# Optimization experiments

Measured on AMD Instinct MI355X. Metric: run time of the kernel, lower is better.

The kernel has to match this reference:

```python
import jax, jax.numpy as jnp
import numpy as np

B, S, D_IN, D_HID, D_OUT = 8, 2048, 1024, 1024, 1024


def setup_inputs() -> dict:
    key = jax.random.key(0)
    ks = jax.random.split(key, 11)
    def lin(kw, kb, fan_in, fan_out):
        bound = 1.0 / np.sqrt(fan_in)
        W = jax.random.uniform(kw, (fan_out, fan_in), minval=-bound, maxval=bound, dtype=jnp.float32)
        b = jax.random.uniform(kb, (fan_out,), minval=-bound, maxval=bound, dtype=jnp.float32)
        return W, b
    Wq, bq = lin(ks[0], ks[1], D_IN, D_HID)
    Wk, bk = lin(ks[2], ks[3], D_IN, D_HID)
    Wv, bv = lin(ks[4], ks[5], D_IN, D_HID)
    Wo, bo = lin(ks[6], ks[7], D_HID, D_OUT)
    gamma = jnp.ones((D_OUT,), jnp.float32)
    beta = jnp.zeros((D_OUT,), jnp.float32)
    x = jax.random.normal(ks[8], (B, S, D_IN), dtype=jnp.float32)
    return {"x": x, "Wq": Wq, "bq": bq, "Wk": Wk, "bk": bk,
            "Wv": Wv, "bv": bv, "Wo": Wo, "bo": bo,
            "gamma": gamma, "beta": beta}


def _layer_norm(x, gamma, beta, eps=1e-5):
    mu = jnp.mean(x, axis=-1, keepdims=True)
    var = jnp.var(x, axis=-1, keepdims=True)
    return (x - mu) * jax.lax.rsqrt(var + eps) * gamma + beta


def reference(x, Wq, bq, Wk, bk, Wv, bv, Wo, bo, gamma, beta):
    q = jnp.einsum('bsd,hd->bsh', x, Wq) + bq   # [B,S,H]
    k = jnp.einsum('bsd,hd->bsh', x, Wk) + bk
    v = jnp.einsum('bsd,hd->bsh', x, Wv) + bv
    scale = 1.0 / jnp.sqrt(jnp.float32(D_HID))
    scores = jnp.einsum('bqh,bkh->bqk', q, k) * scale  # [B,S,S]
    attn = jax.nn.softmax(scores, axis=-1)
    weighted = jnp.einsum('bqk,bkh->bqh', attn, v)     # [B,S,H]
    out = jnp.einsum('bsh,oh->bso', weighted, Wo) + bo # [B,S,O]
    return _layer_norm(out + x, gamma, beta)
```

## Files before the change

### kernel.cpp

```cpp
#include <hip/hip_runtime.h>
#include <hip/hip_bf16.h>
#include <math.h>


typedef __bf16 bf16;
typedef unsigned char u8;
typedef __attribute__((ext_vector_type(8))) __bf16 bf16x8;
typedef __attribute__((ext_vector_type(4))) __bf16 bf16x4;
typedef __attribute__((ext_vector_type(8))) int i32x8;
typedef __attribute__((ext_vector_type(16))) float f32x16;

__device__ __forceinline__ void async16(const u8* g, u8* l) {
    __builtin_amdgcn_global_load_lds(
        (const __attribute__((address_space(1))) void*)g,
        (__attribute__((address_space(3))) void*)l, 16, 0, 0);
}

#define WAITCNT_VM(n) __builtin_amdgcn_s_waitcnt((15 << 8) | (7 << 4) | (n))

__device__ __forceinline__ u8 to_fp8(float v) {
    return (u8)(__builtin_amdgcn_cvt_pk_fp8_f32(v, v, 0, 0) & 0xFF);
}

__global__ __launch_bounds__(256) void cast_f32_fp8(
    const float* __restrict__ in, u8* __restrict__ out, int n)
{
    int i = (blockIdx.x * 256 + threadIdx.x) * 8;
    if (i >= n) return;
    float4 a = *(const float4*)(in + i);
    float4 b = *(const float4*)(in + i + 4);
    int lo = __builtin_amdgcn_cvt_pk_fp8_f32(a.x, a.y, 0, 0);
    lo = __builtin_amdgcn_cvt_pk_fp8_f32(a.z, a.w, lo, 1);
    int hi = __builtin_amdgcn_cvt_pk_fp8_f32(b.x, b.y, 0, 0);
    hi = __builtin_amdgcn_cvt_pk_fp8_f32(b.z, b.w, hi, 1);
    int2 o = { lo, hi };
    *(int2*)(out + i) = o;
}

__global__ __launch_bounds__(256) void cast_w4(
    const float* __restrict__ W0, const float* __restrict__ W1,
    const float* __restrict__ W2, const float* __restrict__ W3,
    u8* __restrict__ out)
{
    const int b = blockIdx.x;
    const int wsel = b >> 9;
    const float* src = (wsel == 0) ? W0 : (wsel == 1) ? W1
                     : (wsel == 2) ? W2 : W3;
    const int i = ((b & 511) * 256 + threadIdx.x) * 8;
    float4 a = *(const float4*)(src + i);
    float4 c = *(const float4*)(src + i + 4);
    int lo = __builtin_amdgcn_cvt_pk_fp8_f32(a.x, a.y, 0, 0);
    lo = __builtin_amdgcn_cvt_pk_fp8_f32(a.z, a.w, lo, 1);
    int hi = __builtin_amdgcn_cvt_pk_fp8_f32(c.x, c.y, 0, 0);
    hi = __builtin_amdgcn_cvt_pk_fp8_f32(c.z, c.w, hi, 1);
    int2 o = { lo, hi };
    *(int2*)(out + (size_t)wsel * 1048576 + i) = o;
}

__global__ __launch_bounds__(512) void gemm_f8(
    const u8* __restrict__ A, long lda, long sA,
    const u8* __restrict__ B, long ldb, long sB,
    void* __restrict__ Cv, long ldc, long sC,
    const float* __restrict__ bias, int bias_mode,
    float scale, int c_mode, int K)
{
    __shared__ u8 lds[3][32768];

    const int gx = gridDim.x, gy = gridDim.y;
    const int slice = gx * gy;
    const int total = slice * gridDim.z;
    int flat = ((int)blockIdx.z * gy + (int)blockIdx.y) * gx + (int)blockIdx.x;
    if ((total & 7) == 0)
        flat = (flat & 7) * (total >> 3) + (flat >> 3);
    const int bz = flat / slice;
    const int rem = flat - bz * slice;
    const int by = rem / gx;
    const int bx = rem - by * gx;

    const int tid = threadIdx.x;
    const long tM = (long)by * 256;
    const long tN = (long)bx * 256;
    A += (long)bz * sA;
    B += (long)bz * sB;

    const int s = tid & 255;
    const int line0 = s >> 3;
    const int sch = (s & 7) ^ (line0 & 7);
    const int skb = (sch & 3) << 4;
    const int srofs = (sch & 4) ? 128 : 0;
    const u8* gsrc;
    long gstr;
    if (tid < 256) { gsrc = A + (tM + line0 + srofs) * lda + skb; gstr = lda; }
    else           { gsrc = B + (tN + line0 + srofs) * ldb + skb; gstr = ldb; }
    const int dbase = ((tid < 256) ? 0 : 16384) + s * 16;

    const int w = tid >> 6, lane = tid & 63;
    const int wr = w >> 2, wc = w & 3;
    const int r32 = lane & 31, kh = lane >> 5;
    const int xr = r32 & 7;

    int oA[4][2], oB[2][2];
    const int cbA = wr * 4;
    const int cbB = (wc >> 1) * 4;
#pragma unroll
    for (int q = 0; q < 4; q++) {
        const int lineA = q * 32 + r32;
        oA[q][0] = lineA * 128 + (((cbA + 2 * kh + 0) ^ xr) << 4);
        oA[q][1] = lineA * 128 + (((cbA + 2 * kh + 1) ^ xr) << 4);
    }
#pragma unroll
    for (int n = 0; n < 2; n++) {
        const int lineB = (wc & 1) * 64 + n * 32 + r32;
        oB[n][0] = 16384 + lineB * 128 + (((cbB + 2 * kh + 0) ^ xr) << 4);
        oB[n][1] = 16384 + lineB * 128 + (((cbB + 2 * kh + 1) ^ xr) << 4);
    }

    f32x16 acc[4][2] = {};

    const int T = K >> 6;

#pragma unroll
    for (int j = 0; j < 4; j++)
        async16(gsrc + (long)j * 32 * gstr, &lds[0][dbase + j * 4096]);
#pragma unroll
    for (int j = 0; j < 4; j++)
        async16(gsrc + 64 + (long)j * 32 * gstr, &lds[1][dbase + j * 4096]);
    WAITCNT_VM(4);
    __builtin_amdgcn_s_barrier();

    union F { i32x8 v; int4 q2[2]; };

    int cur = 0;
    for (int t = 0; t < T; ++t) {
        const u8* cb = lds[cur];
        int nb = cur + 2; if (nb >= 3) nb -= 3;
        u8* pn = lds[nb];
        const long ko = (long)(t + 2) << 6;
        const bool pf = (t + 2 < T);

        F a0, a1, b0, b1;
        a0.q2[0] = *(const int4*)&cb[oA[0][0]];
        a0.q2[1] = *(const int4*)&cb[oA[0][1]];
        a1.q2[0] = *(const int4*)&cb[oA[1][0]];
        a1.q2[1] = *(const int4*)&cb[oA[1][1]];
        b0.q2[0] = *(const int4*)&cb[oB[0][0]];
        b0.q2[1] = *(const int4*)&cb[oB[0][1]];
        b1.q2[0] = *(const int4*)&cb[oB[1][0]];
        b1.q2[1] = *(const int4*)&cb[oB[1][1]];
        if (pf) {
            async16(gsrc + ko,                    pn + dbase);
            async16(gsrc + ko + (long)32 * gstr,  pn + dbase + 4096);
        }
        __builtin_amdgcn_s_barrier();
        asm volatile("s_waitcnt lgkmcnt(0)" ::: "memory");
        __builtin_amdgcn_sched_barrier(0);
        __builtin_amdgcn_s_setprio(1);
        acc[0][0] = __builtin_amdgcn_mfma_scale_f32_32x32x64_f8f6f4(
            a0.v, b0.v, acc[0][0], 0, 0, 0, 0x7F7F7F7F, 0, 0x7F7F7F7F);
        acc[0][1] = __builtin_amdgcn_mfma_scale_f32_32x32x64_f8f6f4(
            a0.v, b1.v, acc[0][1], 0, 0, 0, 0x7F7F7F7F, 0, 0x7F7F7F7F);
        acc[1][0] = __builtin_amdgcn_mfma_scale_f32_32x32x64_f8f6f4(
            a1.v, b0.v, acc[1][0], 0, 0, 0, 0x7F7F7F7F, 0, 0x7F7F7F7F);
        acc[1][1] = __builtin_amdgcn_mfma_scale_f32_32x32x64_f8f6f4(
            a1.v, b1.v, acc[1][1], 0, 0, 0, 0x7F7F7F7F, 0, 0x7F7F7F7F);
        __builtin_amdgcn_s_setprio(0);
        __builtin_amdgcn_s_barrier();

        F a2, a3;
        a2.q2[0] = *(const int4*)&cb[oA[2][0]];
        a2.q2[1] = *(const int4*)&cb[oA[2][1]];
        a3.q2[0] = *(const int4*)&cb[oA[3][0]];
        a3.q2[1] = *(const int4*)&cb[oA[3][1]];
        if (pf) {
            async16(gsrc + ko + (long)64 * gstr,  pn + dbase + 8192);
            async16(gsrc + ko + (long)96 * gstr,  pn + dbase + 12288);
        }
        __builtin_amdgcn_s_barrier();
        asm volatile("s_waitcnt lgkmcnt(0)" ::: "memory");
        __builtin_amdgcn_sched_barrier(0);
        __builtin_amdgcn_s_setprio(1);
        acc[2][0] = __builtin_amdgcn_mfma_scale_f32_32x32x64_f8f6f4(
            a2.v, b0.v, acc[2][0], 0, 0, 0, 0x7F7F7F7F, 0, 0x7F7F7F7F);
        acc[2][1] = __builtin_amdgcn_mfma_scale_f32_32x32x64_f8f6f4(
            a2.v, b1.v, acc[2][1], 0, 0, 0, 0x7F7F7F7F, 0, 0x7F7F7F7F);
        acc[3][0] = __builtin_amdgcn_mfma_scale_f32_32x32x64_f8f6f4(
            a3.v, b0.v, acc[3][0], 0, 0, 0, 0x7F7F7F7F, 0, 0x7F7F7F7F);
        acc[3][1] = __builtin_amdgcn_mfma_scale_f32_32x32x64_f8f6f4(
            a3.v, b1.v, acc[3][1], 0, 0, 0, 0x7F7F7F7F, 0, 0x7F7F7F7F);
        __builtin_amdgcn_s_setprio(0);
        if (pf) WAITCNT_VM(4);
        else if (t + 1 < T) WAITCNT_VM(0);
        __builtin_amdgcn_s_barrier();

        if (++cur >= 3) cur = 0;
    }

#pragma unroll
    for (int q = 0; q < 4; q++) {
#pragma unroll
        for (int n = 0; n < 2; n++) {
            const long gn = tN + wc * 64 + n * 32 + r32;
            const float bn = (bias_mode == 1) ? bias[gn] : 0.0f;
#pragma unroll
            for (int reg = 0; reg < 16; reg++) {
                const int rowf = (reg & 3) + 8 * (reg >> 2) + 4 * kh;
                const long gm = tM + wr * 128 + q * 32 + rowf;
                float v = acc[q][n][reg] * scale + bn;
                if (bias_mode == 2) v += bias[gm];
                if (c_mode == 0)
                    ((bf16*)Cv + (long)bz * sC)[gm * ldc + gn] = (bf16)v;
                else
                    ((u8*)Cv + (long)bz * sC)[gm * ldc + gn] = to_fp8(v);
            }
        }
    }
}

__global__ __launch_bounds__(256) void softmax_f8(
    const bf16* __restrict__ S, u8* __restrict__ P)
{
    const long row = blockIdx.x;
    const bf16* p = S + row * 2048;
    const int t = threadIdx.x;

    bf16x8 v = *(const bf16x8*)(p + t * 8);
    float f[8];
    float m = -3.0e38f;
#pragma unroll
    for (int i = 0; i < 8; i++) { f[i] = (float)v[i]; m = fmaxf(m, f[i]); }
    for (int o = 32; o; o >>= 1) m = fmaxf(m, __shfl_down(m, o));

    __shared__ float sm[4], ssum[4];
    if ((t & 63) == 0) sm[t >> 6] = m;
    __syncthreads();
    m = fmaxf(fmaxf(sm[0], sm[1]), fmaxf(sm[2], sm[3]));

    float s = 0.0f;
#pragma unroll
    for (int i = 0; i < 8; i++) { f[i] = __expf(f[i] - m); s += f[i]; }
    for (int o = 32; o; o >>= 1) s += __shfl_down(s, o);
    if ((t & 63) == 0) ssum[t >> 6] = s;
    __syncthreads();
    s = ssum[0] + ssum[1] + ssum[2] + ssum[3];

    const float c = 256.0f / s;
    int lo = __builtin_amdgcn_cvt_pk_fp8_f32(f[0] * c, f[1] * c, 0, 0);
    lo = __builtin_amdgcn_cvt_pk_fp8_f32(f[2] * c, f[3] * c, lo, 1);
    int hi = __builtin_amdgcn_cvt_pk_fp8_f32(f[4] * c, f[5] * c, 0, 0);
    hi = __builtin_amdgcn_cvt_pk_fp8_f32(f[6] * c, f[7] * c, hi, 1);
    int2 o = { lo, hi };
    *(int2*)(P + row * 2048 + t * 8) = o;
}

__global__ __launch_bounds__(256) void ln_res(
    const bf16* __restrict__ pre, const float* __restrict__ x,
    const float* __restrict__ gamma, const float* __restrict__ beta,
    float* __restrict__ out)
{
    const long row = blockIdx.x;
    const int t = threadIdx.x;
    const long base = row * 1024 + t * 4;

    bf16x4 a = *(const bf16x4*)(pre + base);
    float4 b = *(const float4*)(x + base);
    float v0 = (float)a[0] + b.x, v1 = (float)a[1] + b.y;
    float v2 = (float)a[2] + b.z, v3 = (float)a[3] + b.w;

    float s = v0 + v1 + v2 + v3;
    float q = v0 * v0 + v1 * v1 + v2 * v2 + v3 * v3;
    for (int o = 32; o; o >>= 1) { s += __shfl_down(s, o); q += __shfl_down(q, o); }

    __shared__ float ls[4], lq[4];
    if ((t & 63) == 0) { ls[t >> 6] = s; lq[t >> 6] = q; }
    __syncthreads();
    s = ls[0] + ls[1] + ls[2] + ls[3];
    q = lq[0] + lq[1] + lq[2] + lq[3];

    const float mean = s * (1.0f / 1024.0f);
    const float var = q * (1.0f / 1024.0f) - mean * mean;
    const float rstd = rsqrtf(var + 1e-5f);

    const int c = t * 4;
    float4 g = *(const float4*)(gamma + c);
    float4 be = *(const float4*)(beta + c);
    float4 o;
    o.x = (v0 - mean) * rstd * g.x + be.x;
    o.y = (v1 - mean) * rstd * g.y + be.y;
    o.z = (v2 - mean) * rstd * g.z + be.z;
    o.w = (v3 - mean) * rstd * g.w + be.w;
    *(float4*)(out + base) = o;
}

extern "C" void kernel_launch(void* const* d_in, const int* in_sizes, int n_in,
                              void* d_out, int out_size, void* d_ws, size_t ws_size,
                              hipStream_t stream)
{
    const float* x     = (const float*)d_in[0];
    const float* Wq    = (const float*)d_in[1];
    const float* bq    = (const float*)d_in[2];
    const float* Wk    = (const float*)d_in[3];
    const float* bk    = (const float*)d_in[4];
    const float* Wv    = (const float*)d_in[5];
    const float* bv    = (const float*)d_in[6];
    const float* Wo    = (const float*)d_in[7];
    const float* bo    = (const float*)d_in[8];
    const float* gamma = (const float*)d_in[9];
    const float* beta  = (const float*)d_in[10];
    float* out = (float*)d_out;

    char* ws = (char*)d_ws;
    u8* x8  = (u8*)(ws + (size_t)0);
    u8* Q8  = (u8*)(ws + (size_t)16777216);
    u8* K8  = (u8*)(ws + (size_t)33554432);
    u8* VT8 = (u8*)(ws + (size_t)50331648);
    u8* P8  = (u8*)(ws + (size_t)67108864);
    bf16* Sb = (bf16*)(ws + (size_t)104857600);
    u8* Wq8 = (u8*)(ws + (size_t)176160768);

    cast_f32_fp8<<<8192, 256, 0, stream>>>(x, x8, 16777216);
    cast_w4<<<2048, 256, 0, stream>>>(Wq, Wk, Wv, Wo, Wq8);
    u8* Wk8 = Wq8 + 1048576;
    u8* Wv8 = Wk8 + 1048576;
    u8* Wo8 = Wv8 + 1048576;

    gemm_f8<<<dim3(4, 64, 1), 512, 0, stream>>>(
        x8, 1024, 0, Wq8, 1024, 0, (void*)Q8, 1024, 0, bq, 1, 1.0f, 1, 1024);
    gemm_f8<<<dim3(4, 64, 1), 512, 0, stream>>>(
        x8, 1024, 0, Wk8, 1024, 0, (void*)K8, 1024, 0, bk, 1, 1.0f, 1, 1024);
    gemm_f8<<<dim3(64, 4, 1), 512, 0, stream>>>(
        Wv8, 1024, 0, x8, 1024, 0, (void*)VT8, 16384, 0, bv, 2, 1.0f, 1, 1024);
    gemm_f8<<<dim3(8, 8, 8), 512, 0, stream>>>(
        Q8, 1024, 2097152, K8, 1024, 2097152, (void*)Sb, 2048, 4194304,
        nullptr, 0, 0.03125f, 0, 1024);
    softmax_f8<<<16384, 256, 0, stream>>>(Sb, P8);
    gemm_f8<<<dim3(4, 8, 8), 512, 0, stream>>>(
        P8, 2048, 4194304, VT8, 16384, 2048, (void*)Q8, 1024, 2097152,
        nullptr, 0, 0.0625f, 1, 2048);
    gemm_f8<<<dim3(4, 64, 1), 512, 0, stream>>>(
        Q8, 1024, 0, Wo8, 1024, 0, (void*)Sb, 1024, 0, bo, 1, 0.0625f, 0, 1024);
    ln_res<<<16384, 256, 0, stream>>>((const bf16*)Sb, x, gamma, beta, out);
}
```

Before: 397.9 us.

## Fuse cast kernels, merge Q/K projections, restructure GEMM prefetch pipeline

Merges the x and weight fp8 cast kernels into one launch that also packs bq and bk into a combined bias. Fuses the Q and K projection GEMMs into one GEMM producing an interleaved QK buffer of width 2048, and the scores GEMM now reads it with the matching stride. In the GEMM main loop, the per-iteration barriers drop from four to one, all four prefetch loads are issued together, and the wait on the first half of the LDS reads is relaxed. Fewer launches and barriers cut overhead, but the looser wait counts risk ordering hazards.

```diff
diff --git a/kernel.cpp b/kernel.cpp
--- a/kernel.cpp
+++ b/kernel.cpp
@@ -22,39 +22,46 @@
     return (u8)(__builtin_amdgcn_cvt_pk_fp8_f32(v, v, 0, 0) & 0xFF);
 }
 
-__global__ __launch_bounds__(256) void cast_f32_fp8(
-    const float* __restrict__ in, u8* __restrict__ out, int n)
-{
-    int i = (blockIdx.x * 256 + threadIdx.x) * 8;
-    if (i >= n) return;
-    float4 a = *(const float4*)(in + i);
-    float4 b = *(const float4*)(in + i + 4);
-    int lo = __builtin_amdgcn_cvt_pk_fp8_f32(a.x, a.y, 0, 0);
-    lo = __builtin_amdgcn_cvt_pk_fp8_f32(a.z, a.w, lo, 1);
-    int hi = __builtin_amdgcn_cvt_pk_fp8_f32(b.x, b.y, 0, 0);
-    hi = __builtin_amdgcn_cvt_pk_fp8_f32(b.z, b.w, hi, 1);
-    int2 o = { lo, hi };
-    *(int2*)(out + i) = o;
-}
-
-__global__ __launch_bounds__(256) void cast_w4(
+__global__ __launch_bounds__(256) void cast_all(
+    const float* __restrict__ x,
     const float* __restrict__ W0, const float* __restrict__ W1,
     const float* __restrict__ W2, const float* __restrict__ W3,
-    u8* __restrict__ out)
-{
-    const int b = blockIdx.x;
-    const int wsel = b >> 9;
-    const float* src = (wsel == 0) ? W0 : (wsel == 1) ? W1
-                     : (wsel == 2) ? W2 : W3;
-    const int i = ((b & 511) * 256 + threadIdx.x) * 8;
-    float4 a = *(const float4*)(src + i);
-    float4 c = *(const float4*)(src + i + 4);
-    int lo = __builtin_amdgcn_cvt_pk_fp8_f32(a.x, a.y, 0, 0);
-    lo = __builtin_amdgcn_cvt_pk_fp8_f32(a.z, a.w, lo, 1);
-    int hi = __builtin_amdgcn_cvt_pk_fp8_f32(c.x, c.y, 0, 0);
-    hi = __builtin_amdgcn_cvt_pk_fp8_f32(c.z, c.w, hi, 1);
-    int2 o = { lo, hi };
-    *(int2*)(out + (size_t)wsel * 1048576 + i) = o;
+    const float* __restrict__ bq, const float* __restrict__ bk,
+    u8* __restrict__ x8, u8* __restrict__ w8, float* __restrict__ bqk)
+{
+    const int b = blockIdx.x, t = threadIdx.x;
+    if (b < 8192) {
+        const int i = (b * 256 + t) * 8;
+        float4 a = *(const float4*)(x + i);
+        float4 c = *(const float4*)(x + i + 4);
+        int lo = __builtin_amdgcn_cvt_pk_fp8_f32(a.x, a.y, 0, 0);
+        lo = __builtin_amdgcn_cvt_pk_fp8_f32(a.z, a.w, lo, 1);
+        int hi = __builtin_amdgcn_cvt_pk_fp8_f32(c.x, c.y, 0, 0);
+        hi = __builtin_amdgcn_cvt_pk_fp8_f32(c.z, c.w, hi, 1);
+        int2 o = { lo, hi };
+        *(int2*)(x8 + i) = o;
+    } else if (b < 10240) {
+        const int bb = b - 8192;
+        const int wsel = bb >> 9;
+        const float* src = (wsel == 0) ? W0 : (wsel == 1) ? W1
+                         : (wsel == 2) ? W2 : W3;
+        const int i = ((bb & 511) * 256 + t) * 8;
+        float4 a = *(const float4*)(src + i);
+        float4 c = *(const float4*)(src + i + 4);
+        int lo = __builtin_amdgcn_cvt_pk_fp8_f32(a.x, a.y, 0, 0);
+        lo = __builtin_amdgcn_cvt_pk_fp8_f32(a.z, a.w, lo, 1);
+        int hi = __builtin_amdgcn_cvt_pk_fp8_f32(c.x, c.y, 0, 0);
+        hi = __builtin_amdgcn_cvt_pk_fp8_f32(c.z, c.w, hi, 1);
+        int2 o = { lo, hi };
+        *(int2*)(w8 + (size_t)wsel * 1048576 + i) = o;
+    } else {
+        const int i = t * 8;
+        const float* s = (i < 1024) ? (bq + i) : (bk + i - 1024);
+        float4 a = *(const float4*)s;
+        float4 c = *(const float4*)(s + 4);
+        *(float4*)(bqk + i) = a;
+        *(float4*)(bqk + i + 4) = c;
+    }
 }
 
 __global__ __launch_bounds__(512) void gemm_f8(
@@ -125,18 +132,16 @@
 #pragma unroll
     for (int j = 0; j < 4; j++)
         async16(gsrc + 64 + (long)j * 32 * gstr, &lds[1][dbase + j * 4096]);
-    WAITCNT_VM(4);
-    __builtin_amdgcn_s_barrier();
 
     union F { i32x8 v; int4 q2[2]; };
 
     int cur = 0;
     for (int t = 0; t < T; ++t) {
+        if (t + 1 < T) WAITCNT_VM(4);
+        else WAITCNT_VM(0);
+        __builtin_amdgcn_s_barrier();
+
         const u8* cb = lds[cur];
-        int nb = cur + 2; if (nb >= 3) nb -= 3;
-        u8* pn = lds[nb];
-        const long ko = (long)(t + 2) << 6;
-        const bool pf = (t + 2 < T);
 
         F a0, a1, b0, b1;
         a0.q2[0] = *(const int4*)&cb[oA[0][0]];
@@ -147,12 +152,24 @@
         b0.q2[1] = *(const int4*)&cb[oB[0][1]];
         b1.q2[0] = *(const int4*)&cb[oB[1][0]];
         b1.q2[1] = *(const int4*)&cb[oB[1][1]];
-        if (pf) {
-            async16(gsrc + ko,                    pn + dbase);
-            async16(gsrc + ko + (long)32 * gstr,  pn + dbase + 4096);
+        __builtin_amdgcn_sched_barrier(0);
+
+        F a2, a3;
+        a2.q2[0] = *(const int4*)&cb[oA[2][0]];
+        a2.q2[1] = *(const int4*)&cb[oA[2][1]];
+        a3.q2[0] = *(const int4*)&cb[oA[3][0]];
+        a3.q2[1] = *(const int4*)&cb[oA[3][1]];
+        if (t + 2 < T) {
+            int nb = cur + 2; if (nb >= 3) nb -= 3;
+            u8* pn = lds[nb];
+            const long ko = (long)(t + 2) << 6;
+#pragma unroll
+            for (int j = 0; j < 4; j++)
+                async16(gsrc + ko + (long)j * 32 * gstr,
+                        pn + dbase + j * 4096);
         }
-        __builtin_amdgcn_s_barrier();
-        asm volatile("s_waitcnt lgkmcnt(0)" ::: "memory");
+
+        asm volatile("s_waitcnt lgkmcnt(4)" ::: "memory");
         __builtin_amdgcn_sched_barrier(0);
         __builtin_amdgcn_s_setprio(1);
         acc[0][0] = __builtin_amdgcn_mfma_scale_f32_32x32x64_f8f6f4(
@@ -164,18 +181,7 @@
         acc[1][1] = __builtin_amdgcn_mfma_scale_f32_32x32x64_f8f6f4(
             a1.v, b1.v, acc[1][1], 0, 0, 0, 0x7F7F7F7F, 0, 0x7F7F7F7F);
         __builtin_amdgcn_s_setprio(0);
-        __builtin_amdgcn_s_barrier();
-
-        F a2, a3;
-        a2.q2[0] = *(const int4*)&cb[oA[2][0]];
-        a2.q2[1] = *(const int4*)&cb[oA[2][1]];
-        a3.q2[0] = *(const int4*)&cb[oA[3][0]];
-        a3.q2[1] = *(const int4*)&cb[oA[3][1]];
-        if (pf) {
-            async16(gsrc + ko + (long)64 * gstr,  pn + dbase + 8192);
-            async16(gsrc + ko + (long)96 * gstr,  pn + dbase + 12288);
-        }
-        __builtin_amdgcn_s_barrier();
+
         asm volatile("s_waitcnt lgkmcnt(0)" ::: "memory");
         __builtin_amdgcn_sched_barrier(0);
         __builtin_amdgcn_s_setprio(1);
@@ -188,9 +194,6 @@
         acc[3][1] = __builtin_amdgcn_mfma_scale_f32_32x32x64_f8f6f4(
             a3.v, b1.v, acc[3][1], 0, 0, 0, 0x7F7F7F7F, 0, 0x7F7F7F7F);
         __builtin_amdgcn_s_setprio(0);
-        if (pf) WAITCNT_VM(4);
-        else if (t + 1 < T) WAITCNT_VM(0);
-        __builtin_amdgcn_s_barrier();
 
         if (++cur >= 3) cur = 0;
     }
@@ -310,33 +313,31 @@
 
     char* ws = (char*)d_ws;
     u8* x8  = (u8*)(ws + (size_t)0);
-    u8* Q8  = (u8*)(ws + (size_t)16777216);
-    u8* K8  = (u8*)(ws + (size_t)33554432);
+    u8* QK8 = (u8*)(ws + (size_t)16777216);
     u8* VT8 = (u8*)(ws + (size_t)50331648);
     u8* P8  = (u8*)(ws + (size_t)67108864);
+    float* bqk = (float*)(ws + (size_t)100663296);
     bf16* Sb = (bf16*)(ws + (size_t)104857600);
     u8* Wq8 = (u8*)(ws + (size_t)176160768);
-
-    cast_f32_fp8<<<8192, 256, 0, stream>>>(x, x8, 16777216);
-    cast_w4<<<2048, 256, 0, stream>>>(Wq, Wk, Wv, Wo, Wq8);
-    u8* Wk8 = Wq8 + 1048576;
-    u8* Wv8 = Wk8 + 1048576;
+    u8* Wv8 = Wq8 + 2097152;
     u8* Wo8 = Wv8 + 1048576;
-
-    gemm_f8<<<dim3(4, 64, 1), 512, 0, stream>>>(
-        x8, 1024, 0, Wq8, 1024, 0, (void*)Q8, 1024, 0, bq, 1, 1.0f, 1, 1024);
-    gemm_f8<<<dim3(4, 64, 1), 512, 0, stream>>>(
-        x8, 1024, 0, Wk8, 1024, 0, (void*)K8, 1024, 0, bk, 1, 1.0f, 1, 1024);
+    u8* AO8 = x8;
+
+    cast_all<<<10241, 256, 0, stream>>>(x, Wq, Wk, Wv, Wo, bq, bk,
+                                        x8, Wq8, bqk);
+
+    gemm_f8<<<dim3(8, 64, 1), 512, 0, stream>>>(
+        x8, 1024, 0, Wq8, 1024, 0, (void*)QK8, 2048, 0, bqk, 1, 1.0f, 1, 1024);
     gemm_f8<<<dim3(64, 4, 1), 512, 0, stream>>>(
         Wv8, 1024, 0, x8, 1024, 0, (void*)VT8, 16384, 0, bv, 2, 1.0f, 1, 1024);
     gemm_f8<<<dim3(8, 8, 8), 512, 0, stream>>>(
-        Q8, 1024, 2097152, K8, 1024, 2097152, (void*)Sb, 2048, 4194304,
+        QK8, 2048, 4194304, QK8 + 1024, 2048, 4194304, (void*)Sb, 2048, 4194304,
         nullptr, 0, 0.03125f, 0, 1024);
     softmax_f8<<<16384, 256, 0, stream>>>(Sb, P8);
     gemm_f8<<<dim3(4, 8, 8), 512, 0, stream>>>(
-        P8, 2048, 4194304, VT8, 16384, 2048, (void*)Q8, 1024, 2097152,
+        P8, 2048, 4194304, VT8, 16384, 2048, (void*)AO8, 1024, 2097152,
         nullptr, 0, 0.0625f, 1, 2048);
     gemm_f8<<<dim3(4, 64, 1), 512, 0, stream>>>(
-        Q8, 1024, 0, Wo8, 1024, 0, (void*)Sb, 1024, 0, bo, 1, 0.0625f, 0, 1024);
+        AO8, 1024, 0, Wo8, 1024, 0, (void*)Sb, 1024, 0, bo, 1, 0.0625f, 0, 1024);
     ln_res<<<16384, 256, 0, stream>>>((const bf16*)Sb, x, gamma, beta, out);
 }
```

After: 389.6 us. 2.1% less time.
